# Kernel optimization log

Measured on AMD Instinct MI355X. Metric: run time of the kernel, lower is better.

The kernel has to match this reference:

```python
import jax, jax.numpy as jnp
import numpy as np

C = 256          # in_dim
DQK = C // 16    # query/key channels after 1x1 conv


def setup_inputs() -> dict:
    key = jax.random.key(0)
    ks = jax.random.split(key, 10)
    B, W, H = 8, 64, 64
    s = 0.02
    return {
        "x1": jax.random.normal(ks[0], (B, C, W, H), jnp.float32),
        "x2": jax.random.normal(ks[1], (B, C, W, H), jnp.float32),
        "Wq": jax.random.normal(ks[2], (DQK, 2 * C), jnp.float32) * s,
        "bq": jnp.zeros((DQK,), jnp.float32),
        "Wk": jax.random.normal(ks[3], (DQK, 2 * C), jnp.float32) * s,
        "bk": jnp.zeros((DQK,), jnp.float32),
        "Wv1": jax.random.normal(ks[4], (C, C), jnp.float32) * s,
        "bv1": jnp.zeros((C,), jnp.float32),
        "Wv2": jax.random.normal(ks[5], (C, C), jnp.float32) * s,
        "bv2": jnp.zeros((C,), jnp.float32),
    }


def reference(x1, x2, Wq, bq, Wk, bk, Wv1, bv1, Wv2, bv2):
    B, c, W, H = x1.shape
    N = W * H
    x = jnp.concatenate([x1, x2], axis=1)            # [B, 2C, W, H]
    xf = x.reshape(B, 2 * c, N)                      # flatten spatial
    # 1x1 convs == channel matmuls
    q = jnp.einsum('dc,bcn->bnd', Wq, xf) + bq       # [B, N, DQK]
    k = jnp.einsum('dc,bcn->bdn', Wk, xf) + bk[None, :, None]  # [B, DQK, N]
    energy = jnp.einsum('bnd,bdm->bnm', q, k)        # [B, N, N]
    attention = jax.nn.softmax(energy, axis=-1)
    x1f = x1.reshape(B, c, N)
    x2f = x2.reshape(B, c, N)
    v1 = jnp.einsum('oc,bcn->bon', Wv1, x1f) + bv1[None, :, None]
    v2 = jnp.einsum('oc,bcn->bon', Wv2, x2f) + bv2[None, :, None]
    # bmm(value, attention^T): out[b,c,n] = sum_m v[b,c,m] * attention[b,n,m]
    out1 = jnp.einsum('bcm,bnm->bcn', v1, attention).reshape(B, c, W, H) + x1
    out2 = jnp.einsum('bcm,bnm->bcn', v2, attention).reshape(B, c, W, H) + x2
    return out1, out2, attention
```

## Files before the change

kernel.cpp:

```cpp
#include <hip/hip_runtime.h>
#include <hip/hip_bf16.h>

#define B_ 8
#define C_ 256
#define N_ 4096
#define D_ 16
#define TWO_C 512

typedef __bf16 bf16x8 __attribute__((ext_vector_type(8)));
typedef __bf16 bf16x4 __attribute__((ext_vector_type(4)));
typedef float f32x4 __attribute__((ext_vector_type(4)));
typedef unsigned short u16x4 __attribute__((ext_vector_type(4)));

static __device__ __forceinline__ unsigned short f2bf_rtn(float f) {
    unsigned int u = __builtin_bit_cast(unsigned int, f);
    u += 0x7fffu + ((u >> 16) & 1u);
    return (unsigned short)(u >> 16);
}

__device__ __forceinline__ void gld16(const void* g, void* l) {
    __builtin_amdgcn_global_load_lds(
        (const __attribute__((address_space(1))) unsigned int*)g,
        (__attribute__((address_space(3))) unsigned int*)l, 16, 0, 0);
}

__device__ __forceinline__ f32x4 expv(f32x4 e) {
    f32x4 r = { __expf(e[0]), __expf(e[1]), __expf(e[2]), __expf(e[3]) };
    return r;
}

#define MF(K, Q) __builtin_amdgcn_mfma_f32_16x16x32_bf16((K), (Q), zerov, 0, 0, 0)

__global__ __launch_bounds__(256) void wconv(
    const float* __restrict__ Wv1, const float* __restrict__ Wv2,
    unsigned short* __restrict__ Wbf)
{
    const int i = blockIdx.x * 256 + threadIdx.x;
    f32x4 a = ((const f32x4*)Wv1)[i];
    f32x4 b = ((const f32x4*)Wv2)[i];
    u16x4 ua = { f2bf_rtn(a[0]), f2bf_rtn(a[1]), f2bf_rtn(a[2]), f2bf_rtn(a[3]) };
    u16x4 ub = { f2bf_rtn(b[0]), f2bf_rtn(b[1]), f2bf_rtn(b[2]), f2bf_rtn(b[3]) };
    ((u16x4*)Wbf)[i] = ua;
    ((u16x4*)Wbf)[16384 + i] = ub;
}

__global__ __launch_bounds__(256) void qk_part(
    const float* __restrict__ x1, const float* __restrict__ x2,
    const float* __restrict__ Wq, const float* __restrict__ Wk,
    float* __restrict__ pq, float* __restrict__ pk,
    unsigned short* __restrict__ xbfT)
{
    const int tid = threadIdx.x;
    const int bid = blockIdx.x;
    const int ch = bid & 3;
    const int nt = (bid >> 2) & 15;
    const int b  = bid >> 6;
    const int n  = nt * 256 + tid;

    const float* xs  = (ch < 2) ? x1 : x2;
    const int xoff = (ch & 1) * 128;
    const int wcol = ch * 128;

    const float* px = xs + ((size_t)b * C_ + xoff) * N_ + n;
    unsigned short* xT = xbfT + ((size_t)b * N_ + n) * TWO_C + wcol;

    float aq[D_], ak[D_];
#pragma unroll
    for (int d = 0; d < D_; ++d) { aq[d] = 0.f; ak[d] = 0.f; }

    for (int c8 = 0; c8 < 16; ++c8) {
        unsigned short xb[8];
#pragma unroll
        for (int j = 0; j < 8; ++j) {
            const int c = c8 * 8 + j;
            float xv = px[(size_t)c * N_];
            xb[j] = f2bf_rtn(xv);
#pragma unroll
            for (int d = 0; d < D_; ++d) {
                aq[d] += Wq[d * TWO_C + wcol + c] * xv;
                ak[d] += Wk[d * TWO_C + wcol + c] * xv;
            }
        }
        u16x4 lo = { xb[0], xb[1], xb[2], xb[3] };
        u16x4 hi = { xb[4], xb[5], xb[6], xb[7] };
        *(u16x4*)(xT + c8 * 8)     = lo;
        *(u16x4*)(xT + c8 * 8 + 4) = hi;
    }

    f32x4* q4 = (f32x4*)pq + (size_t)ch * B_ * N_ * 4 + ((size_t)b * N_ + n) * 4;
    f32x4* k4 = (f32x4*)pk + (size_t)ch * B_ * N_ * 4 + ((size_t)b * N_ + n) * 4;
#pragma unroll
    for (int j = 0; j < 4; ++j) {
        f32x4 tq = { aq[4*j], aq[4*j+1], aq[4*j+2], aq[4*j+3] };
        f32x4 tk = { ak[4*j], ak[4*j+1], ak[4*j+2], ak[4*j+3] };
        q4[j] = tq;
        k4[j] = tk;
    }
}

__global__ __launch_bounds__(256) void qk_reduce(
    const float* __restrict__ pq, const float* __restrict__ pk,
    const float* __restrict__ bq, const float* __restrict__ bk,
    unsigned short* __restrict__ qbf, unsigned short* __restrict__ kbf)
{
    const int tg = blockIdx.x * 256 + threadIdx.x;
    const int row = tg >> 2;
    const int d4  = tg & 3;
    const f32x4* pq4 = (const f32x4*)pq;
    const f32x4* pk4 = (const f32x4*)pk;
    f32x4 q = ((const f32x4*)bq)[d4];
    f32x4 k = ((const f32x4*)bk)[d4];
    const size_t stride = (size_t)B_ * N_ * 4;
#pragma unroll
    for (int ch = 0; ch < 4; ++ch) {
        q += pq4[ch * stride + tg];
        k += pk4[ch * stride + tg];
    }
    u16x4 qo = { f2bf_rtn(q[0]), f2bf_rtn(q[1]), f2bf_rtn(q[2]), f2bf_rtn(q[3]) };
    u16x4 ko = { f2bf_rtn(k[0]), f2bf_rtn(k[1]), f2bf_rtn(k[2]), f2bf_rtn(k[3]) };
    u16x4 z  = { 0, 0, 0, 0 };
    *(u16x4*)(qbf + (size_t)row * 32 + d4 * 4)      = qo;
    *(u16x4*)(qbf + (size_t)row * 32 + 16 + d4 * 4) = z;
    *(u16x4*)(kbf + (size_t)row * 32 + d4 * 4)      = ko;
    *(u16x4*)(kbf + (size_t)row * 32 + 16 + d4 * 4) = z;
}

__global__ __launch_bounds__(256) void v_mfma(
    const unsigned short* __restrict__ Wbf,
    const unsigned short* __restrict__ xbfT,
    const float* __restrict__ bv1, const float* __restrict__ bv2,
    unsigned short* __restrict__ vstack)
{
    const int tid  = threadIdx.x;
    const int lane = tid & 63;
    const int wid  = tid >> 6;
    const int bid  = blockIdx.x;
    const int b    = bid >> 7;
    const int half = (bid >> 6) & 1;
    const int n0   = (bid & 63) * 64;
    const int col  = lane & 15;
    const int grp  = lane >> 4;
    const int koff = grp * 8;

    const unsigned short* pa[4];
    const unsigned short* pb[4];
#pragma unroll
    for (int ai = 0; ai < 4; ++ai)
        pa[ai] = Wbf + (size_t)(half * 256 + wid * 64 + ai * 16 + col) * 256 + koff;
#pragma unroll
    for (int bj = 0; bj < 4; ++bj)
        pb[bj] = xbfT + ((size_t)b * N_ + n0 + bj * 16 + col) * TWO_C + half * 256 + koff;

    f32x4 acc[4][4];
#pragma unroll
    for (int ai = 0; ai < 4; ++ai)
#pragma unroll
        for (int bj = 0; bj < 4; ++bj)
            acc[ai][bj] = (f32x4){0.f, 0.f, 0.f, 0.f};

#pragma unroll
    for (int s = 0; s < 8; ++s) {
        bf16x8 af[4], bfr[4];
#pragma unroll
        for (int ai = 0; ai < 4; ++ai) af[ai] = *(const bf16x8*)(pa[ai] + s * 32);
#pragma unroll
        for (int bj = 0; bj < 4; ++bj) bfr[bj] = *(const bf16x8*)(pb[bj] + s * 32);
#pragma unroll
        for (int ai = 0; ai < 4; ++ai)
#pragma unroll
            for (int bj = 0; bj < 4; ++bj)
                acc[ai][bj] = __builtin_amdgcn_mfma_f32_16x16x32_bf16(
                    af[ai], bfr[bj], acc[ai][bj], 0, 0, 0);
    }

    const float* bias = half ? bv2 : bv1;
#pragma unroll
    for (int ai = 0; ai < 4; ++ai) {
        const int cb = wid * 64 + ai * 16 + grp * 4;
#pragma unroll
        for (int r = 0; r < 4; ++r) {
            const float bv = bias[cb + r];
            unsigned short* vr = vstack + ((size_t)b * 512 + half * 256 + cb + r) * N_;
#pragma unroll
            for (int bj = 0; bj < 4; ++bj)
                vr[n0 + bj * 16 + col] = f2bf_rtn(acc[ai][bj][r] + bv);
        }
    }
}

__global__ __launch_bounds__(512) void fused_pv(
    const unsigned short* __restrict__ qbf,
    const unsigned short* __restrict__ kbf,
    const unsigned short* __restrict__ vstack,
    const float* __restrict__ x1, const float* __restrict__ x2,
    float* __restrict__ out1, float* __restrict__ out2,
    float* __restrict__ att)
{
    __shared__ unsigned short Asm[2][256 * 32];
    __shared__ unsigned short Bsm[2][256 * 32];
    __shared__ float sinv[256];

    const int tid  = threadIdx.x;
    const int lane = tid & 63;
    const int wid  = tid >> 6;
    const int wr   = wid >> 2;
    const int wc   = wid & 3;
    const int col  = lane & 15;
    const int grp  = lane >> 4;

    const int bid  = blockIdx.x;
    const int orig = (bid & 7) * 32 + (bid >> 3);
    const int nt = orig & 15;
    const int ct = (orig >> 4) & 1;
    const int b  = orig >> 5;
    const int n0 = nt * 256;

    const f32x4 zerov = {0.f, 0.f, 0.f, 0.f};

    const bf16x8 qf0 = *(const bf16x8*)(qbf + ((size_t)b * N_ + n0 + wid * 32 + col) * 32 + grp * 8);
    const bf16x8 qf1 = *(const bf16x8*)(qbf + ((size_t)b * N_ + n0 + wid * 32 + 16 + col) * 32 + grp * 8);

    const unsigned short* kbase = kbf + ((size_t)b * N_ + col) * 32 + grp * 8;

    float rsum0 = 0.f, rsum1 = 0.f;
    {
        const unsigned short* kq = kbase;
#pragma unroll 2
        for (int T = 0; T < 128; ++T) {
            bf16x8 k0 = *(const bf16x8*)kq;
            bf16x8 k1 = *(const bf16x8*)(kq + 512);
            kq += 1024;
            f32x4 p00 = expv(MF(k0, qf0));
            f32x4 p01 = expv(MF(k1, qf0));
            f32x4 p10 = expv(MF(k0, qf1));
            f32x4 p11 = expv(MF(k1, qf1));
            rsum0 += (p00[0] + p00[1]) + (p00[2] + p00[3])
                   + (p01[0] + p01[1]) + (p01[2] + p01[3]);
            rsum1 += (p10[0] + p10[1]) + (p10[2] + p10[3])
                   + (p11[0] + p11[1]) + (p11[2] + p11[3]);
        }
    }
    rsum0 += __shfl_xor(rsum0, 16); rsum0 += __shfl_xor(rsum0, 32);
    rsum1 += __shfl_xor(rsum1, 16); rsum1 += __shfl_xor(rsum1, 32);
    const float inv0 = 1.f / rsum0;
    const float inv1 = 1.f / rsum1;
    if (lane < 16) {
        sinv[wid * 32 + lane]      = inv0;
        sinv[wid * 32 + 16 + lane] = inv1;
    }

    const unsigned short* Vb = vstack + ((size_t)b * 512 + ct * 256) * N_;
    const int q1 = tid + 512;
    const unsigned short* pa0 = Vb + (size_t)(tid >> 2) * N_ + (((tid & 3) ^ ((tid >> 2) & 3)) * 8);
    const unsigned short* pa1 = Vb + (size_t)(q1 >> 2) * N_ + (((q1 & 3) ^ ((q1 >> 2) & 3)) * 8);

    const int nl0 = wid * 32 + col;
    const int bwA = nl0 * 64 + ((((grp >> 1)) ^ (col & 3)) << 4) + (grp & 1) * 8;
    const int bwB = bwA ^ 32;

    const int raBase = (wr * 128 + col) * 64 + ((grp ^ (col & 3)) << 4);
    const int rbBase = (wc * 64  + col) * 64 + ((grp ^ (col & 3)) << 4);

    float* ars0 = att + (size_t)b * N_ * N_ + (size_t)(n0 + wid * 32 + col) * N_
                + ct * 16 + grp * 4;
    float* ars1 = ars0 + (size_t)16 * N_;

    f32x4 acc[8][4];
#pragma unroll
    for (int ai = 0; ai < 8; ++ai)
#pragma unroll
        for (int bj = 0; bj < 4; ++bj)
            acc[ai][bj] = zerov;

#define PACKB(P, BASE, OFF) do {                                              \
    bf16x4 pkv = { (__bf16)(P)[0], (__bf16)(P)[1],                            \
                   (__bf16)(P)[2], (__bf16)(P)[3] };                          \
    *(bf16x4*)((char*)(BASE) + (OFF)) = pkv;                                  \
} while (0)

    gld16(pa0, &Asm[0][tid * 8]);
    gld16(pa1, &Asm[0][tid * 8 + 4096]);
    pa0 += 32; pa1 += 32;
    __builtin_amdgcn_sched_barrier(0);
    bf16x8 kA0 = *(const bf16x8*)kbase;
    bf16x8 kA1 = *(const bf16x8*)(kbase + 512);
    const unsigned short* kp = kbase + 1024;
    bf16x8 kB0, kB1;
    {
        f32x4 p00 = expv(MF(kA0, qf0));
        f32x4 p01 = expv(MF(kA1, qf0));
        f32x4 p10 = expv(MF(kA0, qf1));
        f32x4 p11 = expv(MF(kA1, qf1));
        kB0 = *(const bf16x8*)kp;
        kB1 = *(const bf16x8*)(kp + 512);
        kp += 1024;
        PACKB(p00, &Bsm[0][0], bwA);
        PACKB(p01, &Bsm[0][0], bwB);
        PACKB(p10, &Bsm[0][0], bwA + 1024);
        PACKB(p11, &Bsm[0][0], bwB + 1024);
        *(f32x4*)ars0 = (ct ? p01 : p00) * inv0;
        *(f32x4*)ars1 = (ct ? p11 : p10) * inv1;
    }
    asm volatile("s_waitcnt vmcnt(4) lgkmcnt(0)" ::: "memory");
    __builtin_amdgcn_s_barrier();
    __builtin_amdgcn_sched_barrier(0);

    auto step = [&](const unsigned short* AsCur, unsigned short* AsNxt,
                    const unsigned short* BsCur, unsigned short* BsNxt,
                    const bf16x8& kc0, const bf16x8& kc1,
                    bf16x8& kn0, bf16x8& kn1, int T, bool doNext) {
        bf16x8 bfr[4], af0[4], af1[4];
#pragma unroll
        for (int bj = 0; bj < 4; ++bj)
            bfr[bj] = *(const bf16x8*)((const char*)BsCur + rbBase + bj * 1024);
#pragma unroll
        for (int ai = 0; ai < 4; ++ai)
            af0[ai] = *(const bf16x8*)((const char*)AsCur + raBase + ai * 1024);
        if (doNext) {
            gld16(pa0, AsNxt + tid * 8);
            gld16(pa1, AsNxt + tid * 8 + 4096);
            pa0 += 32; pa1 += 32;
        }
        __builtin_amdgcn_sched_barrier(0);
        if (doNext) {
            f32x4 p00 = expv(MF(kc0, qf0));
            f32x4 p01 = expv(MF(kc1, qf0));
            f32x4 p10 = expv(MF(kc0, qf1));
            f32x4 p11 = expv(MF(kc1, qf1));
            kn0 = *(const bf16x8*)kp;
            kn1 = *(const bf16x8*)(kp + 512);
            kp += 1024;
            PACKB(p00, BsNxt, bwA);
            PACKB(p01, BsNxt, bwB);
            PACKB(p10, BsNxt, bwA + 1024);
            PACKB(p11, BsNxt, bwB + 1024);
            *(f32x4*)(ars0 + (size_t)T * 32) = (ct ? p01 : p00) * inv0;
            *(f32x4*)(ars1 + (size_t)T * 32) = (ct ? p11 : p10) * inv1;
        }
#pragma unroll
        for (int ai = 0; ai < 4; ++ai)
#pragma unroll
            for (int bj = 0; bj < 4; ++bj)
                acc[ai][bj] = __builtin_amdgcn_mfma_f32_16x16x32_bf16(
                    af0[ai], bfr[bj], acc[ai][bj], 0, 0, 0);
#pragma unroll
        for (int ai = 0; ai < 4; ++ai)
            af1[ai] = *(const bf16x8*)((const char*)AsCur + raBase + (4 + ai) * 1024);
#pragma unroll
        for (int ai = 0; ai < 4; ++ai)
#pragma unroll
            for (int bj = 0; bj < 4; ++bj)
                acc[4 + ai][bj] = __builtin_amdgcn_mfma_f32_16x16x32_bf16(
                    af1[ai], bfr[bj], acc[4 + ai][bj], 0, 0, 0);
        if (doNext) {
            asm volatile("s_waitcnt vmcnt(4) lgkmcnt(0)" ::: "memory");
            __builtin_amdgcn_s_barrier();
            __builtin_amdgcn_sched_barrier(0);
        }
    };

    for (int tt = 0; tt < 64; ++tt) {
        step(&Asm[0][0], &Asm[1][0], &Bsm[0][0], &Bsm[1][0], kB0, kB1, kA0, kA1,
             2 * tt + 1, true);
        step(&Asm[1][0], &Asm[0][0], &Bsm[1][0], &Bsm[0][0], kA0, kA1, kB0, kB1,
             2 * tt + 2, tt < 63);
    }

    __syncthreads();
    float* outp     = ct ? out2 : out1;
    const float* xp = ct ? x2 : x1;
    float sc[4];
#pragma unroll
    for (int bj = 0; bj < 4; ++bj) sc[bj] = sinv[wc * 64 + bj * 16 + col];
#pragma unroll
    for (int ai = 0; ai < 8; ++ai) {
        const int c_l = wr * 128 + ai * 16 + grp * 4;
#pragma unroll
        for (int bj = 0; bj < 4; ++bj) {
            const int n = n0 + wc * 64 + bj * 16 + col;
#pragma unroll
            for (int r = 0; r < 4; ++r) {
                const size_t idx = ((size_t)b * C_ + c_l + r) * N_ + n;
                outp[idx] = acc[ai][bj][r] * sc[bj] + xp[idx];
            }
        }
    }
#undef PACKB
}

extern "C" void kernel_launch(void* const* d_in, const int* in_sizes, int n_in,
                              void* d_out, int out_size, void* d_ws, size_t ws_size,
                              hipStream_t stream)
{
    const float* x1  = (const float*)d_in[0];
    const float* x2  = (const float*)d_in[1];
    const float* Wq  = (const float*)d_in[2];
    const float* bq  = (const float*)d_in[3];
    const float* Wk  = (const float*)d_in[4];
    const float* bk  = (const float*)d_in[5];
    const float* Wv1 = (const float*)d_in[6];
    const float* bv1 = (const float*)d_in[7];
    const float* Wv2 = (const float*)d_in[8];
    const float* bv2 = (const float*)d_in[9];

    float* out  = (float*)d_out;
    float* out1 = out;
    float* out2 = out + (size_t)B_ * C_ * N_;
    float* att  = out + 2 * (size_t)B_ * C_ * N_;

    unsigned short* xbfT = (unsigned short*)att;

    char* ws = (char*)d_ws;
    unsigned short* qbf = (unsigned short*)ws;
    unsigned short* kbf = (unsigned short*)(ws + (size_t)2 * 1024 * 1024);
    unsigned short* vstack = (unsigned short*)(ws + (size_t)4 * 1024 * 1024);
    float* pq = (float*)(ws + (size_t)36 * 1024 * 1024);
    float* pk = (float*)(ws + (size_t)44 * 1024 * 1024);
    unsigned short* Wbf = (unsigned short*)(ws + (size_t)52 * 1024 * 1024);

    wconv<<<64, 256, 0, stream>>>(Wv1, Wv2, Wbf);
    qk_part<<<B_ * 16 * 4, 256, 0, stream>>>(x1, x2, Wq, Wk, pq, pk, xbfT);
    qk_reduce<<<(B_ * N_ * 4) / 256, 256, 0, stream>>>(pq, pk, bq, bk, qbf, kbf);
    v_mfma<<<B_ * 2 * 64, 256, 0, stream>>>(Wbf, xbfT, bv1, bv2, vstack);
    fused_pv<<<256, 512, 0, stream>>>(qbf, kbf, vstack, x1, x2, out1, out2, att);
}
```

Measured before the change: 483.4 us.

## Split softmax row-sum into separate kernel and halve fused_pv query tile

Moves the softmax denominator computation out of fused_pv into a standalone rowsum kernel that writes inverse row sums to workspace. fused_pv now handles 128 query rows per block instead of 256, launching 512 blocks for better CU occupancy, and each block only stores its half of the attention row (split by ct). Each fused_pv block recomputes the exp tile for its rows, so total exp work rises somewhat, and there is one more kernel launch. The per-step MFMA count per block is halved, trading tile reuse for parallelism.

```diff
diff --git a/kernel.cpp b/kernel.cpp
--- a/kernel.cpp
+++ b/kernel.cpp
@@ -188,17 +188,51 @@
     }
 }
 
+__global__ __launch_bounds__(256) void rowsum(
+    const unsigned short* __restrict__ qbf,
+    const unsigned short* __restrict__ kbf,
+    float* __restrict__ sinvbuf)
+{
+    const int tid  = threadIdx.x;
+    const int lane = tid & 63;
+    const int wid  = tid >> 6;
+    const int b  = blockIdx.x >> 6;
+    const int n0 = (blockIdx.x & 63) * 64 + wid * 16;
+    const int col = lane & 15;
+    const int grp = lane >> 4;
+    const f32x4 zerov = {0.f, 0.f, 0.f, 0.f};
+
+    const bf16x8 qf = *(const bf16x8*)(qbf + ((size_t)b * N_ + n0 + col) * 32 + grp * 8);
+    const unsigned short* kp = kbf + ((size_t)b * N_ + col) * 32 + grp * 8;
+
+    float rs = 0.f;
+#pragma unroll 4
+    for (int t = 0; t < 128; ++t) {
+        bf16x8 k0 = *(const bf16x8*)kp;
+        bf16x8 k1 = *(const bf16x8*)(kp + 512);
+        kp += 1024;
+        f32x4 p0 = expv(MF(k0, qf));
+        f32x4 p1 = expv(MF(k1, qf));
+        rs += (p0[0] + p0[1]) + (p0[2] + p0[3])
+            + (p1[0] + p1[1]) + (p1[2] + p1[3]);
+    }
+    rs += __shfl_xor(rs, 16);
+    rs += __shfl_xor(rs, 32);
+    if (lane < 16)
+        sinvbuf[(size_t)b * N_ + n0 + col] = 1.f / rs;
+}
+
 __global__ __launch_bounds__(512) void fused_pv(
     const unsigned short* __restrict__ qbf,
     const unsigned short* __restrict__ kbf,
     const unsigned short* __restrict__ vstack,
+    const float* __restrict__ sinvbuf,
     const float* __restrict__ x1, const float* __restrict__ x2,
     float* __restrict__ out1, float* __restrict__ out2,
     float* __restrict__ att)
 {
     __shared__ unsigned short Asm[2][256 * 32];
-    __shared__ unsigned short Bsm[2][256 * 32];
-    __shared__ float sinv[256];
+    __shared__ unsigned short Bsm[2][128 * 32];
 
     const int tid  = threadIdx.x;
     const int lane = tid & 63;
@@ -209,67 +243,39 @@
     const int grp  = lane >> 4;
 
     const int bid  = blockIdx.x;
-    const int orig = (bid & 7) * 32 + (bid >> 3);
-    const int nt = orig & 15;
-    const int ct = (orig >> 4) & 1;
-    const int b  = orig >> 5;
-    const int n0 = nt * 256;
+    const int orig = (bid & 7) * 64 + (bid >> 3);
+    const int b   = orig >> 6;
+    const int idx = orig & 63;
+    const int ct  = idx >> 5;
+    const int nt  = idx & 31;
+    const int n0  = nt * 128;
 
     const f32x4 zerov = {0.f, 0.f, 0.f, 0.f};
 
-    const bf16x8 qf0 = *(const bf16x8*)(qbf + ((size_t)b * N_ + n0 + wid * 32 + col) * 32 + grp * 8);
-    const bf16x8 qf1 = *(const bf16x8*)(qbf + ((size_t)b * N_ + n0 + wid * 32 + 16 + col) * 32 + grp * 8);
-
+    const int nl = wid * 16 + col;
+    const float invS = sinvbuf[(size_t)b * N_ + n0 + nl];
+
+    const bf16x8 qf = *(const bf16x8*)(qbf + ((size_t)b * N_ + n0 + nl) * 32 + grp * 8);
     const unsigned short* kbase = kbf + ((size_t)b * N_ + col) * 32 + grp * 8;
-
-    float rsum0 = 0.f, rsum1 = 0.f;
-    {
-        const unsigned short* kq = kbase;
-#pragma unroll 2
-        for (int T = 0; T < 128; ++T) {
-            bf16x8 k0 = *(const bf16x8*)kq;
-            bf16x8 k1 = *(const bf16x8*)(kq + 512);
-            kq += 1024;
-            f32x4 p00 = expv(MF(k0, qf0));
-            f32x4 p01 = expv(MF(k1, qf0));
-            f32x4 p10 = expv(MF(k0, qf1));
-            f32x4 p11 = expv(MF(k1, qf1));
-            rsum0 += (p00[0] + p00[1]) + (p00[2] + p00[3])
-                   + (p01[0] + p01[1]) + (p01[2] + p01[3]);
-            rsum1 += (p10[0] + p10[1]) + (p10[2] + p10[3])
-                   + (p11[0] + p11[1]) + (p11[2] + p11[3]);
-        }
-    }
-    rsum0 += __shfl_xor(rsum0, 16); rsum0 += __shfl_xor(rsum0, 32);
-    rsum1 += __shfl_xor(rsum1, 16); rsum1 += __shfl_xor(rsum1, 32);
-    const float inv0 = 1.f / rsum0;
-    const float inv1 = 1.f / rsum1;
-    if (lane < 16) {
-        sinv[wid * 32 + lane]      = inv0;
-        sinv[wid * 32 + 16 + lane] = inv1;
-    }
 
     const unsigned short* Vb = vstack + ((size_t)b * 512 + ct * 256) * N_;
     const int q1 = tid + 512;
     const unsigned short* pa0 = Vb + (size_t)(tid >> 2) * N_ + (((tid & 3) ^ ((tid >> 2) & 3)) * 8);
     const unsigned short* pa1 = Vb + (size_t)(q1 >> 2) * N_ + (((q1 & 3) ^ ((q1 >> 2) & 3)) * 8);
 
-    const int nl0 = wid * 32 + col;
-    const int bwA = nl0 * 64 + ((((grp >> 1)) ^ (col & 3)) << 4) + (grp & 1) * 8;
+    const int bwA = nl * 64 + ((((grp >> 1)) ^ (col & 3)) << 4) + (grp & 1) * 8;
     const int bwB = bwA ^ 32;
 
     const int raBase = (wr * 128 + col) * 64 + ((grp ^ (col & 3)) << 4);
-    const int rbBase = (wc * 64  + col) * 64 + ((grp ^ (col & 3)) << 4);
-
-    float* ars0 = att + (size_t)b * N_ * N_ + (size_t)(n0 + wid * 32 + col) * N_
-                + ct * 16 + grp * 4;
-    float* ars1 = ars0 + (size_t)16 * N_;
-
-    f32x4 acc[8][4];
+    const int rbBase = (wc * 32  + col) * 64 + ((grp ^ (col & 3)) << 4);
+
+    float* ar = att + (size_t)b * N_ * N_ + (size_t)(n0 + nl) * N_ + grp * 4;
+
+    f32x4 acc[8][2];
 #pragma unroll
     for (int ai = 0; ai < 8; ++ai)
 #pragma unroll
-        for (int bj = 0; bj < 4; ++bj)
+        for (int bj = 0; bj < 2; ++bj)
             acc[ai][bj] = zerov;
 
 #define PACKB(P, BASE, OFF) do {                                              \
@@ -282,36 +288,36 @@
     gld16(pa1, &Asm[0][tid * 8 + 4096]);
     pa0 += 32; pa1 += 32;
     __builtin_amdgcn_sched_barrier(0);
-    bf16x8 kA0 = *(const bf16x8*)kbase;
-    bf16x8 kA1 = *(const bf16x8*)(kbase + 512);
-    const unsigned short* kp = kbase + 1024;
-    bf16x8 kB0, kB1;
+    bf16x8 kA0, kA1, kB0, kB1;
+    const unsigned short* kp = kbase;
     {
-        f32x4 p00 = expv(MF(kA0, qf0));
-        f32x4 p01 = expv(MF(kA1, qf0));
-        f32x4 p10 = expv(MF(kA0, qf1));
-        f32x4 p11 = expv(MF(kA1, qf1));
+        bf16x8 k0 = *(const bf16x8*)kp;
+        bf16x8 k1 = *(const bf16x8*)(kp + 512);
+        kp += 1024;
+        f32x4 p0 = expv(MF(k0, qf));
+        f32x4 p1 = expv(MF(k1, qf));
         kB0 = *(const bf16x8*)kp;
         kB1 = *(const bf16x8*)(kp + 512);
         kp += 1024;
-        PACKB(p00, &Bsm[0][0], bwA);
-        PACKB(p01, &Bsm[0][0], bwB);
-        PACKB(p10, &Bsm[0][0], bwA + 1024);
-        PACKB(p11, &Bsm[0][0], bwB + 1024);
-        *(f32x4*)ars0 = (ct ? p01 : p00) * inv0;
-        *(f32x4*)ars1 = (ct ? p11 : p10) * inv1;
-    }
-    asm volatile("s_waitcnt vmcnt(4) lgkmcnt(0)" ::: "memory");
+        PACKB(p0, &Bsm[0][0], bwA);
+        PACKB(p1, &Bsm[0][0], bwB);
+        if (ct == 0) {
+            *(f32x4*)ar        = p0 * invS;
+            *(f32x4*)(ar + 16) = p1 * invS;
+        }
+    }
+    if (ct == 0) asm volatile("s_waitcnt vmcnt(4) lgkmcnt(0)" ::: "memory");
+    else         asm volatile("s_waitcnt vmcnt(2) lgkmcnt(0)" ::: "memory");
     __builtin_amdgcn_s_barrier();
     __builtin_amdgcn_sched_barrier(0);
 
     auto step = [&](const unsigned short* AsCur, unsigned short* AsNxt,
                     const unsigned short* BsCur, unsigned short* BsNxt,
                     const bf16x8& kc0, const bf16x8& kc1,
-                    bf16x8& kn0, bf16x8& kn1, int T, bool doNext) {
-        bf16x8 bfr[4], af0[4], af1[4];
-#pragma unroll
-        for (int bj = 0; bj < 4; ++bj)
+                    bf16x8& kn0, bf16x8& kn1, int Tn, bool doNext) {
+        bf16x8 bfr[2], af0[4], af1[4];
+#pragma unroll
+        for (int bj = 0; bj < 2; ++bj)
             bfr[bj] = *(const bf16x8*)((const char*)BsCur + rbBase + bj * 1024);
 #pragma unroll
         for (int ai = 0; ai < 4; ++ai)
@@ -322,25 +328,26 @@
             pa0 += 32; pa1 += 32;
         }
         __builtin_amdgcn_sched_barrier(0);
+        const bool st = doNext && ((Tn >> 6) == ct);
         if (doNext) {
-            f32x4 p00 = expv(MF(kc0, qf0));
-            f32x4 p01 = expv(MF(kc1, qf0));
-            f32x4 p10 = expv(MF(kc0, qf1));
-            f32x4 p11 = expv(MF(kc1, qf1));
+            f32x4 e0 = MF(kc0, qf);
+            f32x4 e1 = MF(kc1, qf);
             kn0 = *(const bf16x8*)kp;
             kn1 = *(const bf16x8*)(kp + 512);
             kp += 1024;
-            PACKB(p00, BsNxt, bwA);
-            PACKB(p01, BsNxt, bwB);
-            PACKB(p10, BsNxt, bwA + 1024);
-            PACKB(p11, BsNxt, bwB + 1024);
-            *(f32x4*)(ars0 + (size_t)T * 32) = (ct ? p01 : p00) * inv0;
-            *(f32x4*)(ars1 + (size_t)T * 32) = (ct ? p11 : p10) * inv1;
+            f32x4 p0 = expv(e0);
+            f32x4 p1 = expv(e1);
+            PACKB(p0, BsNxt, bwA);
+            PACKB(p1, BsNxt, bwB);
+            if (st) {
+                *(f32x4*)(ar + (size_t)Tn * 32)      = p0 * invS;
+                *(f32x4*)(ar + (size_t)Tn * 32 + 16) = p1 * invS;
+            }
         }
 #pragma unroll
         for (int ai = 0; ai < 4; ++ai)
 #pragma unroll
-            for (int bj = 0; bj < 4; ++bj)
+            for (int bj = 0; bj < 2; ++bj)
                 acc[ai][bj] = __builtin_amdgcn_mfma_f32_16x16x32_bf16(
                     af0[ai], bfr[bj], acc[ai][bj], 0, 0, 0);
 #pragma unroll
@@ -349,11 +356,12 @@
 #pragma unroll
         for (int ai = 0; ai < 4; ++ai)
 #pragma unroll
-            for (int bj = 0; bj < 4; ++bj)
+            for (int bj = 0; bj < 2; ++bj)
                 acc[4 + ai][bj] = __builtin_amdgcn_mfma_f32_16x16x32_bf16(
                     af1[ai], bfr[bj], acc[4 + ai][bj], 0, 0, 0);
         if (doNext) {
-            asm volatile("s_waitcnt vmcnt(4) lgkmcnt(0)" ::: "memory");
+            if (st) asm volatile("s_waitcnt vmcnt(4) lgkmcnt(0)" ::: "memory");
+            else    asm volatile("s_waitcnt vmcnt(2) lgkmcnt(0)" ::: "memory");
             __builtin_amdgcn_s_barrier();
             __builtin_amdgcn_sched_barrier(0);
         }
@@ -366,18 +374,18 @@
              2 * tt + 2, tt < 63);
     }
 
-    __syncthreads();
     float* outp     = ct ? out2 : out1;
     const float* xp = ct ? x2 : x1;
-    float sc[4];
-#pragma unroll
-    for (int bj = 0; bj < 4; ++bj) sc[bj] = sinv[wc * 64 + bj * 16 + col];
+    float sc[2];
+#pragma unroll
+    for (int bj = 0; bj < 2; ++bj)
+        sc[bj] = sinvbuf[(size_t)b * N_ + n0 + wc * 32 + bj * 16 + col];
 #pragma unroll
     for (int ai = 0; ai < 8; ++ai) {
         const int c_l = wr * 128 + ai * 16 + grp * 4;
 #pragma unroll
-        for (int bj = 0; bj < 4; ++bj) {
-            const int n = n0 + wc * 64 + bj * 16 + col;
+        for (int bj = 0; bj < 2; ++bj) {
+            const int n = n0 + wc * 32 + bj * 16 + col;
 #pragma unroll
             for (int r = 0; r < 4; ++r) {
                 const size_t idx = ((size_t)b * C_ + c_l + r) * N_ + n;
@@ -417,10 +425,12 @@
     float* pq = (float*)(ws + (size_t)36 * 1024 * 1024);
     float* pk = (float*)(ws + (size_t)44 * 1024 * 1024);
     unsigned short* Wbf = (unsigned short*)(ws + (size_t)52 * 1024 * 1024);
+    float* sinvbuf = (float*)(ws + (size_t)53 * 1024 * 1024);
 
     wconv<<<64, 256, 0, stream>>>(Wv1, Wv2, Wbf);
     qk_part<<<B_ * 16 * 4, 256, 0, stream>>>(x1, x2, Wq, Wk, pq, pk, xbfT);
     qk_reduce<<<(B_ * N_ * 4) / 256, 256, 0, stream>>>(pq, pk, bq, bk, qbf, kbf);
+    rowsum<<<B_ * 64, 256, 0, stream>>>(qbf, kbf, sinvbuf);
     v_mfma<<<B_ * 2 * 64, 256, 0, stream>>>(Wbf, xbfT, bv1, bv2, vstack);
-    fused_pv<<<256, 512, 0, stream>>>(qbf, kbf, vstack, x1, x2, out1, out2, att);
-}
+    fused_pv<<<512, 512, 0, stream>>>(qbf, kbf, vstack, sinvbuf, x1, x2, out1, out2, att);
+}
```

Result: slower. 526.6 us (+8.9%).
